# Kernel tuning notes

Hardware: AMD Instinct MI355X
Metric: run time of the kernel (lower is better)

The kernel has to match this reference:

```python
import jax, jax.numpy as jnp
import numpy as np

EPS = 1e-5
B, N, NPOINT, K = 16, 4096, 1024, 32
IN_CH, OUT_CH = 64, 64


def index_points(points, idx):
    # points: [B, N, C], idx: [B, ...] -> [B, ..., C]
    b = points.shape[0]
    flat = idx.reshape(b, -1)
    out = jnp.take_along_axis(points, flat[:, :, None], axis=1)
    return out.reshape(idx.shape + (points.shape[-1],))


def bn2d(x, gamma, beta):
    # x: [B, C, H, W], batch-stat BN (training mode), biased variance
    m = x.mean(axis=(0, 2, 3), keepdims=True)
    v = x.var(axis=(0, 2, 3), keepdims=True)
    return gamma[None, :, None, None] * (x - m) / jnp.sqrt(v + EPS) + beta[None, :, None, None]


def bn1d(x, gamma, beta):
    # x: [B, C, L]
    m = x.mean(axis=(0, 2), keepdims=True)
    v = x.var(axis=(0, 2), keepdims=True)
    return gamma[None, :, None] * (x - m) / jnp.sqrt(v + EPS) + beta[None, :, None]


def conv1x1(x, w, b):
    # x: [B, C, H, W], w: [O, C], b: [O]
    return jnp.einsum('bchw,oc->bohw', x, w) + b[None, :, None, None]


def setup_inputs() -> dict:
    key = jax.random.key(0)
    ks = jax.random.split(key, 16)
    inp = {
        'xyz': jax.random.normal(ks[0], (B, N, 3), jnp.float32),
        'points': jax.random.normal(ks[1], (B, N, 61), jnp.float32),
        'local_coordinates': jax.random.normal(ks[2], (B, NPOINT * K, 3), jnp.float32),
        'neighbor_lists': jax.random.randint(ks[3], (B, NPOINT, K), 0, N),
        'data_idx': jax.random.randint(ks[4], (B, NPOINT), 0, N),
        # WeightNet: 3 -> 16 -> 16 -> OUT_CH, each conv1x1 + BN2d + relu
        'w0': jax.random.normal(ks[5], (16, 3), jnp.float32) * 0.1,
        'b0': jnp.zeros((16,), jnp.float32),
        'g0': jnp.ones((16,), jnp.float32),
        'be0': jnp.zeros((16,), jnp.float32),
        'w1': jax.random.normal(ks[6], (16, 16), jnp.float32) * 0.1,
        'b1': jnp.zeros((16,), jnp.float32),
        'g1': jnp.ones((16,), jnp.float32),
        'be1': jnp.zeros((16,), jnp.float32),
        'w2': jax.random.normal(ks[7], (OUT_CH, 16), jnp.float32) * 0.1,
        'b2': jnp.zeros((OUT_CH,), jnp.float32),
        'g2': jnp.ones((OUT_CH,), jnp.float32),
        'be2': jnp.zeros((OUT_CH,), jnp.float32),
        # bn_conv over IN_CH*OUT_CH channels
        'gc': jnp.ones((IN_CH * OUT_CH,), jnp.float32),
        'bc': jnp.zeros((IN_CH * OUT_CH,), jnp.float32),
        # linear IN_CH*OUT_CH -> OUT_CH
        'lw': jax.random.normal(ks[8], (IN_CH * OUT_CH, OUT_CH), jnp.float32) * 0.01,
        'lb': jnp.zeros((OUT_CH,), jnp.float32),
        # bn_linear
        'gl': jnp.ones((OUT_CH,), jnp.float32),
        'bl': jnp.zeros((OUT_CH,), jnp.float32),
    }
    return inp


def reference(xyz, points, local_coordinates, neighbor_lists, data_idx,
              w0, b0, g0, be0, w1, b1, g1, be1, w2, b2, g2, be2,
              gc, bc, lw, lb, gl, bl):
    new_xyz = index_points(xyz, data_idx)                       # [B, NPOINT, 3]
    pts = jnp.concatenate([points, xyz], axis=2)                # [B, N, IN_CH]
    grouped = index_points(pts, neighbor_lists)                 # [B, NPOINT, K, IN_CH]
    grouped = grouped.transpose(0, 1, 3, 2)                     # [B, NPOINT, IN_CH, K]

    # WeightNet on local coordinates
    lc = local_coordinates.reshape(B, NPOINT, K, 3).transpose(0, 3, 2, 1)  # [B, 3, K, NPOINT]
    h = jax.nn.relu(bn2d(conv1x1(lc, w0, b0), g0, be0))
    h = jax.nn.relu(bn2d(conv1x1(h, w1, b1), g1, be1))
    h = jax.nn.relu(bn2d(conv1x1(h, w2, b2), g2, be2))          # [B, OUT_CH, K, NPOINT]
    weights = h.transpose(0, 3, 2, 1)                            # [B, NPOINT, K, OUT_CH]

    # aggregate over neighbors: [B, NPOINT, IN_CH, OUT_CH]
    new_points = jnp.einsum('bnik,bnko->bnio', grouped, weights)
    new_points = new_points.reshape(B, NPOINT, IN_CH * OUT_CH)

    new_points = jax.nn.relu(
        bn1d(new_points.transpose(0, 2, 1), gc, bc).transpose(0, 2, 1))
    new_points = new_points @ lw + lb                            # [B, NPOINT, OUT_CH]
    new_points = bn1d(new_points.transpose(0, 2, 1), gl, bl).transpose(0, 2, 1)
    new_points = jax.nn.relu(new_points)
    return (new_xyz, new_points)
```

## Files before the change

kernel.cpp:

```cpp
#include <hip/hip_runtime.h>
#include <hip/hip_bf16.h>

#define BB 16
#define NN 4096
#define NPOINTS 1024
#define KK 32
#define NPTS (BB*NPOINTS)
#define NWN  (BB*NPOINTS*KK)
#define EPSF 1e-5f
#define SGBLK 512
#define SGIT  4

typedef unsigned short u16;
typedef u16  u16x8 __attribute__((ext_vector_type(8)));
typedef u16  u16x4 __attribute__((ext_vector_type(4)));
typedef short s16x8 __attribute__((ext_vector_type(8)));
typedef float f32x4 __attribute__((ext_vector_type(4)));
typedef float f32x4u __attribute__((ext_vector_type(4), aligned(4)));

__device__ __forceinline__ float bf(u16 u){
  union { unsigned int i; float f; } v; v.i = ((unsigned int)u) << 16; return v.f;
}
__device__ __forceinline__ u16 f2b(float f){
  __hip_bfloat16 h = __float2bfloat16(f);
  union { __hip_bfloat16 hh; u16 u; } v; v.hh = h; return v.u;
}


__global__ __launch_bounds__(256) void k_init(const float* xyz, const int* didx, float* out,
                                              const float* lw, u16* lwbt,
                                              const float* points, u16* ptsw){
  int t = threadIdx.x;
  if (blockIdx.x < 64){
    int p = blockIdx.x * 256 + t;
    int b = p >> 10;
    int idx = didx[p];
    const float* src = xyz + ((size_t)(b * NN + idx)) * 3;
    float* dst = out + (size_t)p * 3;
    dst[0] = src[0]; dst[1] = src[1]; dst[2] = src[2];
  } else if (blockIdx.x < 128){
    __shared__ float T[64][65];
    int ib = blockIdx.x - 64;
    int kb = ib * 64;
    {
      int k = t >> 2, c4 = t & 3;
      #pragma unroll
      for (int j = 0; j < 4; ++j)
        *(f32x4*)&T[k][c4*16 + j*4] = *(const f32x4*)(lw + (size_t)(kb + k)*64 + c4*16 + j*4);
    }
    __syncthreads();
    {
      int n = t >> 2, k4 = t & 3;
      #pragma unroll
      for (int j = 0; j < 16; ++j){
        int k = k4*16 + j;
        lwbt[(size_t)n*4096 + k*64 + ib] = f2b(T[k][n]);
      }
    }
  } else {
    int gid0 = (blockIdx.x - 128) * 256 + t;
    #pragma unroll
    for (int rep = 0; rep < 4; ++rep){
      int idx = gid0 + rep * 131072;
      int row = idx >> 3, c8 = idx & 7;
      const float* prow = points + (size_t)row * 61;
      u16x8 g;
      if (c8 < 7){
        f32x4 lo = *(const f32x4u*)(prow + c8*8);
        f32x4 hi = *(const f32x4u*)(prow + c8*8 + 4);
        g[0]=f2b(lo.x); g[1]=f2b(lo.y); g[2]=f2b(lo.z); g[3]=f2b(lo.w);
        g[4]=f2b(hi.x); g[5]=f2b(hi.y); g[6]=f2b(hi.z); g[7]=f2b(hi.w);
      } else {
        const float* xr = xyz + (size_t)row * 3;
        f32x4 lo = *(const f32x4u*)(prow + 56);
        g[0]=f2b(lo.x); g[1]=f2b(lo.y); g[2]=f2b(lo.z); g[3]=f2b(lo.w);
        g[4]=f2b(prow[60]);
        g[5]=f2b(xr[0]); g[6]=f2b(xr[1]); g[7]=f2b(xr[2]);
      }
      *(u16x8*)(ptsw + (size_t)row*64 + c8*8) = g;
    }
  }
}

__global__ __launch_bounds__(256) void k_stat0(const float* lc, float* PA){
  int t = threadIdx.x;
  float a[9];
  #pragma unroll
  for (int r = 0; r < 9; ++r) a[r] = 0.f;
  size_t base = (size_t)blockIdx.x * 1024 + t;
  for (int ip = 0; ip < 4; ++ip){
    size_t p = base + (size_t)ip * 256;
    float x0 = lc[p*3], x1 = lc[p*3+1], x2 = lc[p*3+2];
    a[0]+=x0; a[1]+=x1; a[2]+=x2;
    a[3]+=x0*x0; a[4]+=x0*x1; a[5]+=x0*x2;
    a[6]+=x1*x1; a[7]+=x1*x2; a[8]+=x2*x2;
  }
  #pragma unroll
  for (int m = 1; m < 64; m <<= 1){
    #pragma unroll
    for (int r = 0; r < 9; ++r) a[r] += __shfl_xor(a[r], m);
  }
  if ((t & 63) == 0){
    float* dst = PA + (size_t)(blockIdx.x*4 + (t>>6)) * 16;
    f32x4 v0 = {a[0],a[1],a[2],a[3]}, v1 = {a[4],a[5],a[6],a[7]}, v2 = {a[8],0.f,0.f,0.f};
    *(f32x4*)dst = v0; *(f32x4*)(dst+4) = v1; *(f32x4*)(dst+8) = v2;
  }
}

__global__ __launch_bounds__(256) void k_red0(const float* PA, const float* w0, const float* b0,
                                              const float* g0, const float* be0, float* F){
  __shared__ float ms[12];
  __shared__ float a0sh[16];
  int t = threadIdx.x;
  if (t < 12){
    float s0=0,s1=0,s2=0,s3=0;
    const float* p = PA + t;
    for (int r = 0; r < 2048; r += 4){
      s0 += p[(size_t)(r+0)*16]; s1 += p[(size_t)(r+1)*16];
      s2 += p[(size_t)(r+2)*16]; s3 += p[(size_t)(r+3)*16];
    }
    ms[t] = (s0+s1)+(s2+s3);
  }
  __syncthreads();
  if (t < 16){
    float wx = w0[t*3], wy = w0[t*3+1], wz = w0[t*3+2], bb = b0[t];
    float lin = wx*ms[0] + wy*ms[1] + wz*ms[2];
    float quad = wx*wx*ms[3] + wy*wy*ms[6] + wz*wz*ms[8]
               + 2.f*(wx*wy*ms[4] + wx*wz*ms[5] + wy*wz*ms[7]);
    float S = lin + (float)NWN * bb;
    float Q = quad + 2.f*bb*lin + (float)NWN*bb*bb;
    float m = S * (1.f/NWN);
    float v = Q * (1.f/NWN) - m*m;
    float a = g0[t] * rsqrtf(v + EPSF);
    float d = be0[t] - m*a;
    a0sh[t] = a;
    F[48+t] = a*bb + d;
  }
  __syncthreads();
  if (t < 48) F[t] = a0sh[t/3] * w0[t];
}

__global__ __launch_bounds__(256) void k_statG1(const float* lc, const float* F, float* PB){
  __shared__ f32x4 w0p[16];
  __shared__ __align__(16) u16 Ht[4][16*72];
  __shared__ float GS[4][16][17];
  __shared__ float SHs[4][16];
  int t = threadIdx.x;
  int w = t >> 6, l = t & 63;
  if (t < 16){
    f32x4 wv = {F[t*3], F[t*3+1], F[t*3+2], F[48+t]};
    w0p[t] = wv;
  }
  __syncthreads();
  f32x4 acc = {0.f,0.f,0.f,0.f};
  float sh[16];
  #pragma unroll
  for (int r = 0; r < 16; ++r) sh[r] = 0.f;
  u16* Hw = &Ht[w][0];
  for (int it = 0; it < SGIT; ++it){
    size_t p = (size_t)blockIdx.x * (SGIT*256) + (size_t)it*256 + w*64 + l;
    float x0 = lc[p*3], x1 = lc[p*3+1], x2 = lc[p*3+2];
    float h[16];
    #pragma unroll
    for (int oc = 0; oc < 16; ++oc){
      f32x4 wv = w0p[oc];
      h[oc] = fmaxf(0.f, wv.x*x0 + wv.y*x1 + wv.z*x2 + wv.w);
      sh[oc] += h[oc];
    }
    #pragma unroll
    for (int c = 0; c < 16; ++c) Hw[c*72 + l] = f2b(h[c]);
    __syncthreads();
    #pragma unroll
    for (int tt = 0; tt < 2; ++tt){
      s16x8 af = *(const s16x8*)&Hw[(l & 15)*72 + tt*32 + (l >> 4)*8];
      acc = __builtin_amdgcn_mfma_f32_16x16x32_bf16(af, af, acc, 0, 0, 0);
    }
    __syncthreads();
  }
  #pragma unroll
  for (int r = 0; r < 4; ++r)
    GS[w][(l>>4)*4 + r][l & 15] = acc[r];
  #pragma unroll
  for (int m = 1; m < 64; m <<= 1){
    #pragma unroll
    for (int r = 0; r < 16; ++r) sh[r] += __shfl_xor(sh[r], m);
  }
  if (l == 0){
    #pragma unroll
    for (int r = 0; r < 16; ++r) SHs[w][r] = sh[r];
  }
  __syncthreads();
  {
    int i = t >> 4, j = t & 15;
    float g = GS[0][i][j] + GS[1][i][j] + GS[2][i][j] + GS[3][i][j];
    PB[(size_t)blockIdx.x*272 + t] = g;
    if (t < 16)
      PB[(size_t)blockIdx.x*272 + 256 + t] = SHs[0][t]+SHs[1][t]+SHs[2][t]+SHs[3][t];
  }
}

__global__ __launch_bounds__(256) void k_statG2(const float* lc, const float* F,
                                                const u16* w1Bg, float* PB){
  __shared__ f32x4 w0p[16];
  __shared__ __align__(16) u16 Ht0[4][64*40];
  __shared__ __align__(16) u16 Ht1[4][16*72];
  __shared__ float GS[4][16][17];
  __shared__ float SHs[4][16];
  int t = threadIdx.x;
  int w = t >> 6, l = t & 63;
  if (t < 16){
    f32x4 wv = {F[t*3], F[t*3+1], F[t*3+2], F[48+t]};
    w0p[t] = wv;
  }
  s16x8 w1B = *(const s16x8*)&w1Bg[l*8];
  float b1f = F[320 + (l & 15)];
  u16* H0w = &Ht0[w][0];
  u16* H1w = &Ht1[w][0];
  {
    u16x8 z8 = {0,0,0,0,0,0,0,0};
    *(u16x8*)&H0w[l*40 + 16] = z8;
    *(u16x8*)&H0w[l*40 + 24] = z8;
  }
  __syncthreads();
  f32x4 acc = {0.f,0.f,0.f,0.f};
  float shloc = 0.f;
  for (int it = 0; it < SGIT; ++it){
    size_t p = (size_t)blockIdx.x * (SGIT*256) + (size_t)it*256 + w*64 + l;
    float x0 = lc[p*3], x1 = lc[p*3+1], x2 = lc[p*3+2];
    u16x8 p0, p1;
    #pragma unroll
    for (int oc = 0; oc < 8; ++oc){
      f32x4 wv = w0p[oc];
      p0[oc] = f2b(fmaxf(0.f, wv.x*x0 + wv.y*x1 + wv.z*x2 + wv.w));
    }
    #pragma unroll
    for (int oc = 0; oc < 8; ++oc){
      f32x4 wv = w0p[8+oc];
      p1[oc] = f2b(fmaxf(0.f, wv.x*x0 + wv.y*x1 + wv.z*x2 + wv.w));
    }
    *(u16x8*)&H0w[l*40]     = p0;
    *(u16x8*)&H0w[l*40 + 8] = p1;
    __syncthreads();
    #pragma unroll
    for (int mt = 0; mt < 4; ++mt){
      s16x8 af = *(const s16x8*)&H0w[(mt*16 + (l & 15))*40 + (l >> 4)*8];
      f32x4 c = {b1f, b1f, b1f, b1f};
      c = __builtin_amdgcn_mfma_f32_16x16x32_bf16(af, w1B, c, 0, 0, 0);
      #pragma unroll
      for (int r = 0; r < 4; ++r){
        float v = fmaxf(0.f, c[r]);
        shloc += v;
        H1w[(l & 15)*72 + mt*16 + (l >> 4)*4 + r] = f2b(v);
      }
    }
    __syncthreads();
    #pragma unroll
    for (int tt = 0; tt < 2; ++tt){
      s16x8 afg = *(const s16x8*)&H1w[(l & 15)*72 + tt*32 + (l >> 4)*8];
      acc = __builtin_amdgcn_mfma_f32_16x16x32_bf16(afg, afg, acc, 0, 0, 0);
    }
    __syncthreads();
  }
  #pragma unroll
  for (int r = 0; r < 4; ++r)
    GS[w][(l>>4)*4 + r][l & 15] = acc[r];
  shloc += __shfl_xor(shloc, 16);
  shloc += __shfl_xor(shloc, 32);
  if (l < 16) SHs[w][l] = shloc;
  __syncthreads();
  {
    int i = t >> 4, j = t & 15;
    float g = GS[0][i][j] + GS[1][i][j] + GS[2][i][j] + GS[3][i][j];
    PB[(size_t)blockIdx.x*272 + t] = g;
    if (t < 16)
      PB[(size_t)blockIdx.x*272 + 256 + t] = SHs[0][t]+SHs[1][t]+SHs[2][t]+SHs[3][t];
  }
}

__global__ __launch_bounds__(256) void k_red1(const float* PB, const float* w1, const float* b1,
                                              const float* g1, const float* be1, float* F,
                                              u16* w1Bg){
  __shared__ float red[272];
  __shared__ float a1sh[16];
  int t = threadIdx.x;
  for (int e = t; e < 272; e += 256){
    float s = 0.f;
    for (int r = 0; r < SGBLK; ++r) s += PB[(size_t)r*272 + e];
    red[e] = s;
  }
  __syncthreads();
  if (t < 16){
    float wv[16];
    #pragma unroll
    for (int ic = 0; ic < 16; ++ic) wv[ic] = w1[t*16+ic];
    float lin = 0.f;
    #pragma unroll
    for (int ic = 0; ic < 16; ++ic) lin += wv[ic]*red[256+ic];
    float quad = 0.f;
    for (int i = 0; i < 16; ++i){
      float ri = 0.f;
      #pragma unroll
      for (int j = 0; j < 16; ++j) ri += wv[j]*red[i*16+j];
      quad += wv[i]*ri;
    }
    float bb = b1[t];
    float S = lin + (float)NWN * bb;
    float Q = quad + 2.f*bb*lin + (float)NWN*bb*bb;
    float m = S * (1.f/NWN);
    float v = Q * (1.f/NWN) - m*m;
    float a = g1[t] * rsqrtf(v + EPSF);
    float d = be1[t] - m*a;
    a1sh[t] = a;
    F[320+t] = a*bb + d;
  }
  __syncthreads();
  F[64 + t] = a1sh[t >> 4] * w1[t];
  if (t < 64){
    int oc = t & 15, icb = (t >> 4) * 8;
    u16x8 fr;
    #pragma unroll
    for (int j = 0; j < 8; ++j){
      int ic = icb + j;
      fr[j] = (ic < 16) ? f2b(a1sh[oc] * w1[oc*16 + ic]) : (u16)0;
    }
    *(u16x8*)&w1Bg[t*8] = fr;
  }
}

__global__ __launch_bounds__(256) void k_red2(const float* PB, const float* w2, const float* b2,
                                              const float* g2, const float* be2, float* F,
                                              u16* w2Bg){
  __shared__ float red[272];
  __shared__ float a2sh[64];
  int t = threadIdx.x;
  for (int e = t; e < 272; e += 256){
    float s = 0.f;
    for (int r = 0; r < SGBLK; ++r) s += PB[(size_t)r*272 + e];
    red[e] = s;
  }
  __syncthreads();
  if (t < 64){
    float wv[16];
    #pragma unroll
    for (int ic = 0; ic < 16; ++ic) wv[ic] = w2[t*16+ic];
    float lin = 0.f;
    #pragma unroll
    for (int ic = 0; ic < 16; ++ic) lin += wv[ic]*red[256+ic];
    float quad = 0.f;
    for (int i = 0; i < 16; ++i){
      float ri = 0.f;
      #pragma unroll
      for (int j = 0; j < 16; ++j) ri += wv[j]*red[i*16+j];
      quad += wv[i]*ri;
    }
    float bb = b2[t];
    float S = lin + (float)NWN * bb;
    float Q = quad + 2.f*bb*lin + (float)NWN*bb*bb;
    float m = S * (1.f/NWN);
    float v = Q * (1.f/NWN) - m*m;
    float a = g2[t] * rsqrtf(v + EPSF);
    float d = be2[t] - m*a;
    a2sh[t] = a;
    F[1360+t] = a*bb + d;
  }
  __syncthreads();
  for (int i = t; i < 1024; i += 256) F[336+i] = a2sh[i >> 4] * w2[i];
  {
    int ot = t >> 6, lane = t & 63;
    int oc = ot*16 + (lane & 15), icb = ((lane >> 4)) * 8;
    u16x8 fr;
    #pragma unroll
    for (int j = 0; j < 8; ++j){
      int ic = icb + j;
      fr[j] = (ic < 16) ? f2b(a2sh[oc] * w2[oc*16 + ic]) : (u16)0;
    }
    *(u16x8*)&w2Bg[t*8] = fr;
  }
}

__global__ __launch_bounds__(256) void k_main(const float* lcg, const int* nbrg,
    const u16* ptsw, const float* F,
    const u16* w1Bg, const u16* w2Bg,
    u16* npw){
  __shared__ __align__(16) u16 Gr[2][64*40];
  __shared__ __align__(16) u16 WrBuf[2][64*40];
  __shared__ __align__(16) u16 H1bf[2][32*40];
  int t = threadIdx.x;
  int w = t >> 6, l = t & 63;
  int p0 = blockIdx.x * 2;
  s16x8 w1B  = *(const s16x8*)&w1Bg[l*8];
  s16x8 w2B0 = *(const s16x8*)&w2Bg[(0*64 + l)*8];
  s16x8 w2B1 = *(const s16x8*)&w2Bg[(1*64 + l)*8];
  s16x8 w2B2 = *(const s16x8*)&w2Bg[(2*64 + l)*8];
  s16x8 w2B3 = *(const s16x8*)&w2Bg[(3*64 + l)*8];
  float b1f  = F[320 + (l & 15)];
  float b2f0 = F[1360 +  0 + (l & 15)];
  float b2f1 = F[1360 + 16 + (l & 15)];
  float b2f2 = F[1360 + 32 + (l & 15)];
  float b2f3 = F[1360 + 48 + (l & 15)];
  int oc0 = (t & 7) * 2;
  f32x4 w0a = {F[oc0*3], F[oc0*3+1], F[oc0*3+2], F[48+oc0]};
  f32x4 w0b = {F[oc0*3+3], F[oc0*3+4], F[oc0*3+5], F[48+oc0+1]};
  {
    int k = t >> 3, c = 16 + (t & 7)*2;
    *(unsigned int*)&WrBuf[0][k*40 + c] = 0u;
    *(unsigned int*)&WrBuf[1][k*40 + c] = 0u;
    *(unsigned int*)&H1bf[0][k*40 + c] = 0u;
    *(unsigned int*)&H1bf[1][k*40 + c] = 0u;
  }
  {
    int kg = w*8 + (l >> 3), c8 = l & 7;
    int kphys = ((w ^ (c8 & 3)) << 3) + (l >> 3);
    #pragma unroll
    for (int pt = 0; pt < 2; ++pt){
      int point = p0 + pt;
      int bbp = point >> 10;
      int n = nbrg[(size_t)point*32 + kg];
      u16x8 g = *(const u16x8*)(ptsw + (size_t)(bbp * NN + n)*64 + c8*8);
      #pragma unroll
      for (int j = 0; j < 8; ++j)
        Gr[pt][(c8*8 + j)*40 + kphys] = g[j];
    }
  }
  {
    int k = t >> 3;
    #pragma unroll
    for (int pt = 0; pt < 2; ++pt){
      const float* xp = lcg + (size_t)(p0 + pt)*96 + k*3;
      float x0 = xp[0], x1 = xp[1], x2 = xp[2];
      WrBuf[pt][k*40 + oc0]     = f2b(fmaxf(0.f, w0a.x*x0 + w0a.y*x1 + w0a.z*x2 + w0a.w));
      WrBuf[pt][k*40 + oc0 + 1] = f2b(fmaxf(0.f, w0b.x*x0 + w0b.y*x1 + w0b.z*x2 + w0b.w));
    }
  }
  __syncthreads();
  {
    int pt = w >> 1, kt = w & 1;
    s16x8 af = *(const s16x8*)&WrBuf[pt][(kt*16 + (l & 15))*40 + (l >> 4)*8];
    f32x4 acc = {b1f, b1f, b1f, b1f};
    acc = __builtin_amdgcn_mfma_f32_16x16x32_bf16(af, w1B, acc, 0, 0, 0);
    #pragma unroll
    for (int r = 0; r < 4; ++r)
      H1bf[pt][(kt*16 + (l >> 4)*4 + r)*40 + (l & 15)] = f2b(fmaxf(0.f, acc[r]));
  }
  __syncthreads();
  {
    int pt = w & 1, kt = w >> 1;
    s16x8 af = *(const s16x8*)&H1bf[pt][(kt*16 + (l & 15))*40 + (l >> 4)*8];
    int kbase = kt*16 + (l >> 4)*4;
    f32x4 a0c = {b2f0,b2f0,b2f0,b2f0};
    a0c = __builtin_amdgcn_mfma_f32_16x16x32_bf16(af, w2B0, a0c, 0, 0, 0);
    u16x4 s0v; s0v[0]=f2b(fmaxf(0.f,a0c[0])); s0v[1]=f2b(fmaxf(0.f,a0c[1]));
    s0v[2]=f2b(fmaxf(0.f,a0c[2])); s0v[3]=f2b(fmaxf(0.f,a0c[3]));
    *(u16x4*)&WrBuf[pt][( 0 + (l & 15))*40 + kbase] = s0v;
    f32x4 a1c = {b2f1,b2f1,b2f1,b2f1};
    a1c = __builtin_amdgcn_mfma_f32_16x16x32_bf16(af, w2B1, a1c, 0, 0, 0);
    u16x4 s1v; s1v[0]=f2b(fmaxf(0.f,a1c[0])); s1v[1]=f2b(fmaxf(0.f,a1c[1]));
    s1v[2]=f2b(fmaxf(0.f,a1c[2])); s1v[3]=f2b(fmaxf(0.f,a1c[3]));
    *(u16x4*)&WrBuf[pt][(16 + (l & 15))*40 + kbase] = s1v;
    f32x4 a2c = {b2f2,b2f2,b2f2,b2f2};
    a2c = __builtin_amdgcn_mfma_f32_16x16x32_bf16(af, w2B2, a2c, 0, 0, 0);
    u16x4 s2v; s2v[0]=f2b(fmaxf(0.f,a2c[0])); s2v[1]=f2b(fmaxf(0.f,a2c[1]));
    s2v[2]=f2b(fmaxf(0.f,a2c[2])); s2v[3]=f2b(fmaxf(0.f,a2c[3]));
    *(u16x4*)&WrBuf[pt][(32 + (l & 15))*40 + kbase] = s2v;
    f32x4 a3c = {b2f3,b2f3,b2f3,b2f3};
    a3c = __builtin_amdgcn_mfma_f32_16x16x32_bf16(af, w2B3, a3c, 0, 0, 0);
    u16x4 s3v; s3v[0]=f2b(fmaxf(0.f,a3c[0])); s3v[1]=f2b(fmaxf(0.f,a3c[1]));
    s3v[2]=f2b(fmaxf(0.f,a3c[2])); s3v[3]=f2b(fmaxf(0.f,a3c[3]));
    *(u16x4*)&WrBuf[pt][(48 + (l & 15))*40 + kbase] = s3v;
  }
  __syncthreads();
  {
    int li = l & 15, lkb = l >> 4, lr = (l >> 4) * 4;
    #pragma unroll
    for (int pt = 0; pt < 2; ++pt){
      s16x8 bfrag = *(const s16x8*)&WrBuf[pt][(w*16 + li)*40 + lkb*8];
      size_t obase = (size_t)(p0 + pt)*4096 + (size_t)(w*16 + li)*64 + lr;
      #pragma unroll
      for (int it = 0; it < 4; ++it){
        int ch = it*16 + li;
        int key = (ch >> 3) & 3;
        s16x8 afrag = *(const s16x8*)&Gr[pt][ch*40 + ((lkb ^ key) << 3)];
        f32x4 z = {0.f, 0.f, 0.f, 0.f};
        f32x4 d = __builtin_amdgcn_mfma_f32_16x16x32_bf16(afrag, bfrag, z, 0, 0, 0);
        u16x4 st;
        st[0] = f2b(d[0]); st[1] = f2b(d[1]); st[2] = f2b(d[2]); st[3] = f2b(d[3]);
        *(u16x4*)(npw + obase + it*16) = st;
      }
    }
  }
}

__global__ __launch_bounds__(256) void k_statC(const u16* npw, float* PC){
  int t = threadIdx.x;
  float s[16], q[16];
  #pragma unroll
  for (int j = 0; j < 16; ++j){ s[j] = 0.f; q[j] = 0.f; }
  size_t rowbase = (size_t)blockIdx.x * 64;
  for (int p = 0; p < 64; ++p){
    const u16* row = npw + (rowbase + p) * 4096 + t * 16;
    u16x8 a = *(const u16x8*)row;
    u16x8 b = *(const u16x8*)(row + 8);
    #pragma unroll
    for (int j = 0; j < 8; ++j){ float v = bf(a[j]); s[j]   += v; q[j]   += v*v; }
    #pragma unroll
    for (int j = 0; j < 8; ++j){ float v = bf(b[j]); s[8+j] += v; q[8+j] += v*v; }
  }
  float* dst = PC + (size_t)blockIdx.x * 8192 + t * 16;
  #pragma unroll
  for (int j = 0; j < 16; ++j){ dst[j] = s[j]; dst[4096 + j] = q[j]; }
}

__global__ __launch_bounds__(256) void k_finC(const float* PC, const float* gc, const float* bc,
                                              float* AC, float* DC){
  int qpos = blockIdx.x * 256 + threadIdx.x;
  float s = 0.f, q = 0.f;
  for (int r = 0; r < 256; ++r){
    s += PC[(size_t)r * 8192 + qpos];
    q += PC[(size_t)r * 8192 + 4096 + qpos];
  }
  int ch = (qpos & 63)*64 + (qpos >> 6);
  float m = s * (1.f/16384.f);
  float v = q * (1.f/16384.f) - m*m;
  float a = gc[ch] * rsqrtf(v + EPSF);
  AC[qpos] = a; DC[qpos] = bc[ch] - m*a;
}

__global__ __launch_bounds__(256) void k_linear(const u16* npw, const float* AC, const float* DC,
                                                const u16* lwbt, const float* lb, float* yw,
                                                float* PL){
  __shared__ u16 Al[16*72];
  __shared__ u16 Bl[64*72];
  __shared__ float cps[64], cpq[64];
  int t = threadIdx.x;
  int w = t >> 6, l = t & 63;
  int rowbase = blockIdx.x * 16;
  int rA = t >> 4, cA = t & 15;
  int nB = t >> 3, cB = t & 7;
  const u16* Aptr = npw + (size_t)(rowbase + rA)*4096 + cA*4;
  const u16* B0ptr = lwbt + (size_t)nB*4096 + cB*8;
  const u16* B1ptr = lwbt + (size_t)(nB + 32)*4096 + cB*8;
  f32x4 acc0 = {0.f,0.f,0.f,0.f};
  u16x4 uA  = *(const u16x4*)(Aptr);
  u16x8 uB0 = *(const u16x8*)(B0ptr);
  u16x8 uB1 = *(const u16x8*)(B1ptr);
  for (int kb = 0; kb < 4096; kb += 64){
    __syncthreads();
    {
      int kk = kb + cA*4;
      f32x4 av = *(const f32x4*)(AC + kk);
      f32x4 dv = *(const f32x4*)(DC + kk);
      u16x4 o;
      o[0] = f2b(fmaxf(0.f, av.x*bf(uA[0]) + dv.x));
      o[1] = f2b(fmaxf(0.f, av.y*bf(uA[1]) + dv.y));
      o[2] = f2b(fmaxf(0.f, av.z*bf(uA[2]) + dv.z));
      o[3] = f2b(fmaxf(0.f, av.w*bf(uA[3]) + dv.w));
      *(u16x4*)&Al[rA*72 + cA*4] = o;
      *(u16x8*)&Bl[nB*72 + cB*8]        = uB0;
      *(u16x8*)&Bl[(nB + 32)*72 + cB*8] = uB1;
    }
    if (kb + 64 < 4096){
      uA  = *(const u16x4*)(Aptr + kb + 64);
      uB0 = *(const u16x8*)(B0ptr + kb + 64);
      uB1 = *(const u16x8*)(B1ptr + kb + 64);
    }
    __syncthreads();
    #pragma unroll
    for (int ks = 0; ks < 2; ++ks){
      s16x8 af  = *(const s16x8*)&Al[((l & 15))*72 + ks*32 + (l >> 4)*8];
      s16x8 bf0 = *(const s16x8*)&Bl[(w*16 + (l & 15))*72 + ks*32 + (l >> 4)*8];
      acc0 = __builtin_amdgcn_mfma_f32_16x16x32_bf16(af, bf0, acc0, 0, 0, 0);
    }
  }
  int col0 = w*16 + (l & 15);
  float lb0 = lb[col0];
  float s0 = 0.f, q0 = 0.f;
  if (t < 64){ cps[t] = 0.f; cpq[t] = 0.f; }
  __syncthreads();
  #pragma unroll
  for (int r = 0; r < 4; ++r){
    int row = rowbase + (l >> 4)*4 + r;
    float y0 = acc0[r] + lb0;
    yw[(size_t)row*64 + col0] = y0;
    s0 += y0; q0 += y0*y0;
  }
  atomicAdd(&cps[col0], s0); atomicAdd(&cpq[col0], q0);
  __syncthreads();
  if (t < 64){
    PL[blockIdx.x*128 + t]      = cps[t];
    PL[blockIdx.x*128 + 64 + t] = cpq[t];
  }
}

__global__ __launch_bounds__(128) void k_redF(const float* PL, float* SL){
  int t = threadIdx.x;
  float s = 0.f;
  for (int b = 0; b < 1024; ++b) s += PL[b*128 + t];
  SL[t] = s;
}

__global__ __launch_bounds__(256) void k_final(const float* yw, const float* SL,
                                               const float* gl, const float* bl, float* out){
  int e = (blockIdx.x * 256 + threadIdx.x) * 4;
  int o = e & 63;
  f32x4 y = *(const f32x4*)(yw + e);
  f32x4 r;
  #pragma unroll
  for (int j = 0; j < 4; ++j){
    float m = SL[o+j] * (1.f/16384.f);
    float v = SL[64+o+j] * (1.f/16384.f) - m*m;
    float a = gl[o+j] * rsqrtf(v + EPSF);
    float d = bl[o+j] - m*a;
    r[j] = fmaxf(0.f, a*y[j] + d);
  }
  *(f32x4*)(out + 49152 + e) = r;
}

extern "C" void kernel_launch(void* const* d_in, const int* in_sizes, int n_in,
                              void* d_out, int out_size, void* d_ws, size_t ws_size,
                              hipStream_t stream){
  (void)in_sizes; (void)n_in; (void)out_size; (void)ws_size;
  const float* xyz    = (const float*)d_in[0];
  const float* points = (const float*)d_in[1];
  const float* lc     = (const float*)d_in[2];
  const int*   nbrl   = (const int*)d_in[3];
  const int*   didx   = (const int*)d_in[4];
  const float* w0 = (const float*)d_in[5];
  const float* b0 = (const float*)d_in[6];
  const float* g0 = (const float*)d_in[7];
  const float* be0= (const float*)d_in[8];
  const float* w1 = (const float*)d_in[9];
  const float* b1 = (const float*)d_in[10];
  const float* g1 = (const float*)d_in[11];
  const float* be1= (const float*)d_in[12];
  const float* w2 = (const float*)d_in[13];
  const float* b2 = (const float*)d_in[14];
  const float* g2 = (const float*)d_in[15];
  const float* be2= (const float*)d_in[16];
  const float* gc = (const float*)d_in[17];
  const float* bc = (const float*)d_in[18];
  const float* lw = (const float*)d_in[19];
  const float* lb = (const float*)d_in[20];
  const float* gl = (const float*)d_in[21];
  const float* bl = (const float*)d_in[22];
  float* out = (float*)d_out;
  char* ws = (char*)d_ws;

  float* F   = (float*)ws;
  float* SL  = F + 1536;
  float* AC  = SL + 128;
  float* DC  = AC + 4096;
  float* PA  = DC + 4096;
  float* PB1 = PA + 32768;
  float* PB2 = PB1 + 139264;
  float* PL  = PB2 + 139264;
  u16*  w1Bg = (u16*)(PL + 131072);
  u16*  w2Bg = w1Bg + 512;
  float* PC  = (float*)(ws + 4194304);
  u16*  npw  = (u16*)(ws + 4194304 + 8388608);
  float* yw  = (float*)(ws + 4194304 + 8388608 + 134217728);
  u16*  lwbt = (u16*)(ws + 4194304 + 8388608 + 134217728 + 4194304);
  u16*  ptsw = (u16*)(ws + 4194304 + 8388608 + 134217728 + 4194304 + 1048576);

  k_init  <<<640,   256, 0, stream>>>(xyz, didx, out, lw, lwbt, points, ptsw);
  k_stat0 <<<512,   256, 0, stream>>>(lc, PA);
  k_red0  <<<1,     256, 0, stream>>>(PA, w0, b0, g0, be0, F);
  k_statG1<<<SGBLK, 256, 0, stream>>>(lc, F, PB1);
  k_red1  <<<1,     256, 0, stream>>>(PB1, w1, b1, g1, be1, F, w1Bg);
  k_statG2<<<SGBLK, 256, 0, stream>>>(lc, F, w1Bg, PB2);
  k_red2  <<<1,     256, 0, stream>>>(PB2, w2, b2, g2, be2, F, w2Bg);
  k_main  <<<8192,  256, 0, stream>>>(lc, nbrl, ptsw, F, w1Bg, w2Bg, npw);
  k_statC <<<256,   256, 0, stream>>>(npw, PC);
  k_finC  <<<16,    256, 0, stream>>>(PC, gc, bc, AC, DC);
  k_linear<<<1024,  256, 0, stream>>>(npw, AC, DC, lwbt, lb, yw, PL);
  k_redF  <<<1,     128, 0, stream>>>(PL, SL);
  k_final <<<1024,  256, 0, stream>>>(yw, SL, gl, bl, out);
}
```

Measured before the change: 259.1 us.

## Merge stat0 into init kernel and double-buffer LDS in k_linear

Folds the first local-coordinate statistics pass into the k_init launch as extra blocks, removing one kernel launch and letting it overlap with the gather/transpose work. Separately, k_linear now double-buffers its A/B tiles in shared memory, so the next tile is staged while MFMAs consume the current one. This cuts the loop to one barrier per iteration. It costs twice the LDS per block, which could lower occupancy slightly.

```diff
diff --git a/kernel.cpp b/kernel.cpp
--- a/kernel.cpp
+++ b/kernel.cpp
@@ -29,7 +29,8 @@
 
 __global__ __launch_bounds__(256) void k_init(const float* xyz, const int* didx, float* out,
                                               const float* lw, u16* lwbt,
-                                              const float* points, u16* ptsw){
+                                              const float* points, u16* ptsw,
+                                              const float* lc, float* PA){
   int t = threadIdx.x;
   if (blockIdx.x < 64){
     int p = blockIdx.x * 256 + t;
@@ -57,7 +58,7 @@
         lwbt[(size_t)n*4096 + k*64 + ib] = f2b(T[k][n]);
       }
     }
-  } else {
+  } else if (blockIdx.x < 640){
     int gid0 = (blockIdx.x - 128) * 256 + t;
     #pragma unroll
     for (int rep = 0; rep < 4; ++rep){
@@ -79,31 +80,29 @@
       }
       *(u16x8*)(ptsw + (size_t)row*64 + c8*8) = g;
     }
-  }
-}
-
-__global__ __launch_bounds__(256) void k_stat0(const float* lc, float* PA){
-  int t = threadIdx.x;
-  float a[9];
-  #pragma unroll
-  for (int r = 0; r < 9; ++r) a[r] = 0.f;
-  size_t base = (size_t)blockIdx.x * 1024 + t;
-  for (int ip = 0; ip < 4; ++ip){
-    size_t p = base + (size_t)ip * 256;
-    float x0 = lc[p*3], x1 = lc[p*3+1], x2 = lc[p*3+2];
-    a[0]+=x0; a[1]+=x1; a[2]+=x2;
-    a[3]+=x0*x0; a[4]+=x0*x1; a[5]+=x0*x2;
-    a[6]+=x1*x1; a[7]+=x1*x2; a[8]+=x2*x2;
-  }
-  #pragma unroll
-  for (int m = 1; m < 64; m <<= 1){
-    #pragma unroll
-    for (int r = 0; r < 9; ++r) a[r] += __shfl_xor(a[r], m);
-  }
-  if ((t & 63) == 0){
-    float* dst = PA + (size_t)(blockIdx.x*4 + (t>>6)) * 16;
-    f32x4 v0 = {a[0],a[1],a[2],a[3]}, v1 = {a[4],a[5],a[6],a[7]}, v2 = {a[8],0.f,0.f,0.f};
-    *(f32x4*)dst = v0; *(f32x4*)(dst+4) = v1; *(f32x4*)(dst+8) = v2;
+  } else {
+    int bid = blockIdx.x - 640;
+    float a[9];
+    #pragma unroll
+    for (int r = 0; r < 9; ++r) a[r] = 0.f;
+    size_t base = (size_t)bid * 1024 + t;
+    for (int ip = 0; ip < 4; ++ip){
+      size_t p = base + (size_t)ip * 256;
+      float x0 = lc[p*3], x1 = lc[p*3+1], x2 = lc[p*3+2];
+      a[0]+=x0; a[1]+=x1; a[2]+=x2;
+      a[3]+=x0*x0; a[4]+=x0*x1; a[5]+=x0*x2;
+      a[6]+=x1*x1; a[7]+=x1*x2; a[8]+=x2*x2;
+    }
+    #pragma unroll
+    for (int m = 1; m < 64; m <<= 1){
+      #pragma unroll
+      for (int r = 0; r < 9; ++r) a[r] += __shfl_xor(a[r], m);
+    }
+    if ((t & 63) == 0){
+      float* dst = PA + (size_t)(bid*4 + (t>>6)) * 16;
+      f32x4 v0 = {a[0],a[1],a[2],a[3]}, v1 = {a[4],a[5],a[6],a[7]}, v2 = {a[8],0.f,0.f,0.f};
+      *(f32x4*)dst = v0; *(f32x4*)(dst+4) = v1; *(f32x4*)(dst+8) = v2;
+    }
   }
 }
 
@@ -528,25 +527,42 @@
 __global__ __launch_bounds__(256) void k_linear(const u16* npw, const float* AC, const float* DC,
                                                 const u16* lwbt, const float* lb, float* yw,
                                                 float* PL){
-  __shared__ u16 Al[16*72];
-  __shared__ u16 Bl[64*72];
+  __shared__ u16 Al[2][16*72];
+  __shared__ u16 Bl[2][64*72];
   __shared__ float cps[64], cpq[64];
   int t = threadIdx.x;
   int w = t >> 6, l = t & 63;
   int rowbase = blockIdx.x * 16;
   int rA = t >> 4, cA = t & 15;
   int nB = t >> 3, cB = t & 7;
-  const u16* Aptr = npw + (size_t)(rowbase + rA)*4096 + cA*4;
+  const u16* Aptr  = npw  + (size_t)(rowbase + rA)*4096 + cA*4;
   const u16* B0ptr = lwbt + (size_t)nB*4096 + cB*8;
   const u16* B1ptr = lwbt + (size_t)(nB + 32)*4096 + cB*8;
   f32x4 acc0 = {0.f,0.f,0.f,0.f};
   u16x4 uA  = *(const u16x4*)(Aptr);
   u16x8 uB0 = *(const u16x8*)(B0ptr);
   u16x8 uB1 = *(const u16x8*)(B1ptr);
+  {
+    int kk = cA*4;
+    f32x4 av = *(const f32x4*)(AC + kk);
+    f32x4 dv = *(const f32x4*)(DC + kk);
+    u16x4 o;
+    o[0] = f2b(fmaxf(0.f, av.x*bf(uA[0]) + dv.x));
+    o[1] = f2b(fmaxf(0.f, av.y*bf(uA[1]) + dv.y));
+    o[2] = f2b(fmaxf(0.f, av.z*bf(uA[2]) + dv.z));
+    o[3] = f2b(fmaxf(0.f, av.w*bf(uA[3]) + dv.w));
+    *(u16x4*)&Al[0][rA*72 + cA*4] = o;
+    *(u16x8*)&Bl[0][nB*72 + cB*8]        = uB0;
+    *(u16x8*)&Bl[0][(nB + 32)*72 + cB*8] = uB1;
+  }
+  uA  = *(const u16x4*)(Aptr + 64);
+  uB0 = *(const u16x8*)(B0ptr + 64);
+  uB1 = *(const u16x8*)(B1ptr + 64);
+  __syncthreads();
+  int cur = 0;
   for (int kb = 0; kb < 4096; kb += 64){
-    __syncthreads();
-    {
-      int kk = kb + cA*4;
+    if (kb + 64 < 4096){
+      int kk = kb + 64 + cA*4;
       f32x4 av = *(const f32x4*)(AC + kk);
       f32x4 dv = *(const f32x4*)(DC + kk);
       u16x4 o;
@@ -554,22 +570,23 @@
       o[1] = f2b(fmaxf(0.f, av.y*bf(uA[1]) + dv.y));
       o[2] = f2b(fmaxf(0.f, av.z*bf(uA[2]) + dv.z));
       o[3] = f2b(fmaxf(0.f, av.w*bf(uA[3]) + dv.w));
-      *(u16x4*)&Al[rA*72 + cA*4] = o;
-      *(u16x8*)&Bl[nB*72 + cB*8]        = uB0;
-      *(u16x8*)&Bl[(nB + 32)*72 + cB*8] = uB1;
-    }
-    if (kb + 64 < 4096){
-      uA  = *(const u16x4*)(Aptr + kb + 64);
-      uB0 = *(const u16x8*)(B0ptr + kb + 64);
-      uB1 = *(const u16x8*)(B1ptr + kb + 64);
+      *(u16x4*)&Al[cur^1][rA*72 + cA*4] = o;
+      *(u16x8*)&Bl[cur^1][nB*72 + cB*8]        = uB0;
+      *(u16x8*)&Bl[cur^1][(nB + 32)*72 + cB*8] = uB1;
+      if (kb + 128 < 4096){
+        uA  = *(const u16x4*)(Aptr + kb + 128);
+        uB0 = *(const u16x8*)(B0ptr + kb + 128);
+        uB1 = *(const u16x8*)(B1ptr + kb + 128);
+      }
+    }
+    #pragma unroll
+    for (int ks = 0; ks < 2; ++ks){
+      s16x8 af  = *(const s16x8*)&Al[cur][((l & 15))*72 + ks*32 + (l >> 4)*8];
+      s16x8 bf0 = *(const s16x8*)&Bl[cur][(w*16 + (l & 15))*72 + ks*32 + (l >> 4)*8];
+      acc0 = __builtin_amdgcn_mfma_f32_16x16x32_bf16(af, bf0, acc0, 0, 0, 0);
     }
     __syncthreads();
-    #pragma unroll
-    for (int ks = 0; ks < 2; ++ks){
-      s16x8 af  = *(const s16x8*)&Al[((l & 15))*72 + ks*32 + (l >> 4)*8];
-      s16x8 bf0 = *(const s16x8*)&Bl[(w*16 + (l & 15))*72 + ks*32 + (l >> 4)*8];
-      acc0 = __builtin_amdgcn_mfma_f32_16x16x32_bf16(af, bf0, acc0, 0, 0, 0);
-    }
+    cur ^= 1;
   }
   int col0 = w*16 + (l & 15);
   float lb0 = lb[col0];
@@ -661,8 +678,7 @@
   u16*  lwbt = (u16*)(ws + 4194304 + 8388608 + 134217728 + 4194304);
   u16*  ptsw = (u16*)(ws + 4194304 + 8388608 + 134217728 + 4194304 + 1048576);
 
-  k_init  <<<640,   256, 0, stream>>>(xyz, didx, out, lw, lwbt, points, ptsw);
-  k_stat0 <<<512,   256, 0, stream>>>(lc, PA);
+  k_init  <<<1152,  256, 0, stream>>>(xyz, didx, out, lw, lwbt, points, ptsw, lc, PA);
   k_red0  <<<1,     256, 0, stream>>>(PA, w0, b0, g0, be0, F);
   k_statG1<<<SGBLK, 256, 0, stream>>>(lc, F, PB1);
   k_red1  <<<1,     256, 0, stream>>>(PB1, w1, b1, g1, be1, F, w1Bg);
```

Result: no change. 257.9 us (-0.5%).
